# Kernel tuning notes

Measured on AMD Instinct MI355X. Metric: run time of the kernel, lower is better.

Reference implementation:

```python
import jax, jax.numpy as jnp
from jax import lax
import numpy as np

WIN_SIZE = 11
WIN_SIGMA = 1.5
DATA_RANGE = 1.0
K1, K2 = 0.01, 0.03
DN = ('NCHW', 'OIHW', 'NCHW')


def _gauss_1d(size, sigma):
    coords = jnp.arange(size, dtype=jnp.float32) - (size // 2)
    g = jnp.exp(-coords ** 2 / (2.0 * sigma ** 2))
    return g / g.sum()


def _gaussian_filter(x, g):
    # depthwise separable valid conv: along W then along H (order irrelevant)
    C = x.shape[1]
    kw = jnp.tile(g.reshape(1, 1, 1, -1), (C, 1, 1, 1))  # [C,1,1,K]
    kh = jnp.tile(g.reshape(1, 1, -1, 1), (C, 1, 1, 1))  # [C,1,K,1]
    x = lax.conv_general_dilated(x, kw, (1, 1), 'VALID',
                                 feature_group_count=C, dimension_numbers=DN)
    x = lax.conv_general_dilated(x, kh, (1, 1), 'VALID',
                                 feature_group_count=C, dimension_numbers=DN)
    return x


def setup_inputs() -> dict:
    key = jax.random.key(0)
    k1, k2 = jax.random.split(key)
    X = jax.random.uniform(k1, (32, 3, 512, 512), dtype=jnp.float32, minval=-1.0, maxval=1.0)
    Y = jax.random.uniform(k2, (32, 3, 512, 512), dtype=jnp.float32, minval=-1.0, maxval=1.0)
    return {"X": X, "Y": Y}


def reference(X, Y):
    # channel == 3 -> normalize from [-1,1] to [0,1]
    X = (X + 1.0) / 2.0
    Y = (Y + 1.0) / 2.0

    g = _gauss_1d(WIN_SIZE, WIN_SIGMA).astype(X.dtype)
    C1 = (K1 * DATA_RANGE) ** 2
    C2 = (K2 * DATA_RANGE) ** 2

    mu1 = _gaussian_filter(X, g)
    mu2 = _gaussian_filter(Y, g)
    mu1_sq = mu1 * mu1
    mu2_sq = mu2 * mu2
    mu1_mu2 = mu1 * mu2

    sigma1_sq = _gaussian_filter(X * X, g) - mu1_sq
    sigma2_sq = _gaussian_filter(Y * Y, g) - mu2_sq
    sigma12 = _gaussian_filter(X * Y, g) - mu1_mu2

    cs_map = (2.0 * sigma12 + C2) / (sigma1_sq + sigma2_sq + C2)
    ssim_map = (2.0 * mu1_mu2 + C1) / (mu1_sq + mu2_sq + C1) * cs_map

    # size_average=True, full=False -> scalar mean SSIM
    return ssim_map.mean()
```

## Files before the change

### kernel.cpp

```cpp
#include <hip/hip_runtime.h>
#include <cmath>


#define HH 512
#define WW 512
#define OH 502
#define OW 502
#define NC 96
#define TXS 32
#define TYB 30
#define INR 40
#define INRS 42
#define RAWP 13
#define NRAW (INR*RAWP)
#define HP4 33
#define GX 16
#define GY 17
#define NSLOT 64

typedef float f4 __attribute__((ext_vector_type(4)));

struct GaussW { float g[11]; };

static __device__ __forceinline__ f4 sp(float s) { return (f4){s, s, s, s}; }

__global__ __launch_bounds__(256, 4) void ssim_kernel(
        const float* __restrict__ X, const float* __restrict__ Y,
        double* __restrict__ acc, GaussW gw) {
    __shared__ f4 rawS[2 * NRAW];
    __shared__ f4 hS[INRS][HP4];
    __shared__ double wsum[4];

    const int tid = threadIdx.x;
    const int R0 = blockIdx.y * TYB;
    const int C0 = blockIdx.x * TXS;
    const float* Xp = X + (size_t)blockIdx.z * (HH * WW);
    const float* Yp = Y + (size_t)blockIdx.z * (HH * WW);

    #pragma unroll
    for (int k = 0; k < 5; ++k) {
        int i = (k << 8) + tid;
        if (i < 2 * NRAW) {
            int a  = i >= NRAW;
            int j  = a ? i - NRAW : i;
            int r  = j / RAWP;
            int c4 = j - r * RAWP;
            const float* bp  = a ? Yp : Xp;
            const float* src = bp + min(R0 + r, HH - 1) * WW
                                  + min(C0 + 4 * c4, WW - 4);
            f4* dst = &rawS[i & ~63];
            __builtin_amdgcn_global_load_lds(
                (const __attribute__((address_space(1))) void*)src,
                (__attribute__((address_space(3))) void*)dst, 16, 0, 0);
        }
    }
    __syncthreads();

    auto task = [&](int r, int cg) {
        const int ib = RAWP * r + cg;
        f4 x0 = rawS[ib + 0], x1 = rawS[ib + 1];
        f4 x2 = rawS[ib + 2], x3 = rawS[ib + 3];
        f4 y0 = rawS[NRAW + ib + 0], y1 = rawS[NRAW + ib + 1];
        f4 y2 = rawS[NRAW + ib + 2], y3 = rawS[NRAW + ib + 3];
        float xv[16], yv[16];
        #pragma unroll
        for (int i = 0; i < 4; ++i) {
            xv[i] = x0[i]; xv[4 + i] = x1[i]; xv[8 + i] = x2[i]; xv[12 + i] = x3[i];
            yv[i] = y0[i]; yv[4 + i] = y1[i]; yv[8 + i] = y2[i]; yv[12 + i] = y3[i];
        }
        f4 a0v = sp(0.f), a1v = sp(0.f), a2v = sp(0.f), a3v = sp(0.f);
        #pragma unroll
        for (int k = 0; k < 14; ++k) {
            float x = xv[k], y = yv[k];
            f4 P;
            P.x = x; P.y = y;
            P.z = fmaf(x, x, y * y);
            P.w = x * y;
            #pragma unroll
            for (int j = 0; j < 4; ++j) {
                int u = k - j;
                if (u >= 0 && u < 11) {
                    f4 G = sp(gw.g[u]);
                    if (j == 0) a0v = __builtin_elementwise_fma(G, P, a0v);
                    if (j == 1) a1v = __builtin_elementwise_fma(G, P, a1v);
                    if (j == 2) a2v = __builtin_elementwise_fma(G, P, a2v);
                    if (j == 3) a3v = __builtin_elementwise_fma(G, P, a3v);
                }
            }
        }
        hS[r][4 * cg + 0] = a0v;
        hS[r][4 * cg + 1] = a1v;
        hS[r][4 * cg + 2] = a2v;
        hS[r][4 * cg + 3] = a3v;
    };
    {
        const int cg = (tid >> 3) & 7;
        task((tid & 7) | ((tid >> 6) << 3), cg);
        if (tid < 64) task((tid & 7) | 32, cg);
    }
    __syncthreads();

    const int c  = tid & 31;
    const int rb = (tid >> 5) * 4;
    f4 A[4];
    #pragma unroll
    for (int j = 0; j < 4; ++j) A[j] = sp(0.f);
    #pragma unroll
    for (int k = 0; k < 14; ++k) {
        f4 v = hS[rb + k][c];
        #pragma unroll
        for (int j = 0; j < 4; ++j) {
            int u = k - j;
            if (u >= 0 && u < 11) {
                f4 G = sp(gw.g[u]);
                A[j] = __builtin_elementwise_fma(G, v, A[j]);
            }
        }
    }

    const float C1 = 1.0e-4f;
    const float C2 = 9.0e-4f;
    float nn[4], dd[4];
    #pragma unroll
    for (int j = 0; j < 4; ++j) {
        f4 v = A[j];
        float t1 = v.x + 1.f, t2 = v.y + 1.f;
        float num1 = fmaf(t1 * t2, 0.5f, C1);
        float den1 = fmaf(fmaf(t2, t2, t1 * t1), 0.25f, C1);
        float num2 = fmaf(v.w - v.x * v.y, 0.5f, C2);
        float den2 = fmaf(v.z - fmaf(v.x, v.x, v.y * v.y), 0.25f, C2);
        bool valid = (rb + j < TYB) & (R0 + rb + j < OH) & (C0 + c < OW);
        nn[j] = valid ? num1 * num2 : 0.f;
        dd[j] = valid ? den1 * den2 : 1.f;
    }
    float d01 = dd[0] * dd[1], d23 = dd[2] * dd[3];
    float s01 = fmaf(nn[0], dd[1], nn[1] * dd[0]);
    float s23 = fmaf(nn[2], dd[3], nn[3] * dd[2]);
    double tsum = (double)(fmaf(s01, d23, s23 * d01) / (d01 * d23));

    #pragma unroll
    for (int off = 32; off > 0; off >>= 1)
        tsum += __shfl_down(tsum, off, 64);
    if ((tid & 63) == 0) wsum[tid >> 6] = tsum;
    __syncthreads();
    if (tid == 0) {
        int slot = (blockIdx.x + blockIdx.y * GX + blockIdx.z * GX * GY) & (NSLOT - 1);
        atomicAdd(&acc[slot * 8], wsum[0] + wsum[1] + wsum[2] + wsum[3]);
    }
}

__global__ void ssim_finalize(const double* __restrict__ acc,
                              float* __restrict__ out) {
    int lane = threadIdx.x;
    double t = acc[lane * 8];
    #pragma unroll
    for (int off = 32; off > 0; off >>= 1)
        t += __shfl_down(t, off, 64);
    if (lane == 0)
        out[0] = (float)(t * (1.0 / (double)((long long)NC * OH * OW)));
}

extern "C" void kernel_launch(void* const* d_in, const int* in_sizes, int n_in,
                              void* d_out, int out_size, void* d_ws, size_t ws_size,
                              hipStream_t stream) {
    const float* X = (const float*)d_in[0];
    const float* Y = (const float*)d_in[1];
    float* out = (float*)d_out;
    double* acc = (double*)d_ws;

    hipMemsetAsync(d_ws, 0, NSLOT * 64, stream);

    GaussW gw;
    {
        double g[11], s = 0.0;
        for (int i = 0; i < 11; ++i) {
            double d = (double)(i - 5);
            g[i] = exp(-d * d / (2.0 * 1.5 * 1.5));
            s += g[i];
        }
        for (int i = 0; i < 11; ++i) gw.g[i] = (float)(g[i] / s);
    }

    dim3 grid(GX, GY, NC);
    ssim_kernel<<<grid, dim3(256), 0, stream>>>(X, Y, acc, gw);
    ssim_finalize<<<1, dim3(64), 0, stream>>>(acc, out);
}
```

Before: 261.7 us.

## Stream column strips through persistent blocks with double-buffered DMA and ring-buffered halo

Each block now walks down a whole 32-column strip of one image in 16 iterations instead of handling a single 30-row tile. Raw rows are double-buffered through LDS with async global-to-LDS loads for the next batch issued while the current batch is filtered. A circular horizontal-result buffer keeps the 10-row halo between iterations, so overlapping input rows are no longer reloaded and re-filtered. This cuts redundant halo traffic and the halo horizontal pass, but the grid shrinks from 16x17x96 to 16x96 blocks, which lowers parallelism, and each iteration adds barriers.

```diff
diff --git a/kernel.cpp b/kernel.cpp
--- a/kernel.cpp
+++ b/kernel.cpp
@@ -8,14 +8,13 @@
 #define OW 502
 #define NC 96
 #define TXS 32
-#define TYB 30
-#define INR 40
-#define INRS 42
+#define BROWS 32
+#define NIT 16
+#define RAWR 64
 #define RAWP 13
-#define NRAW (INR*RAWP)
+#define HSR 48
 #define HP4 33
 #define GX 16
-#define GY 17
 #define NSLOT 64
 
 typedef float f4 __attribute__((ext_vector_type(4)));
@@ -23,50 +22,59 @@
 struct GaussW { float g[11]; };
 
 static __device__ __forceinline__ f4 sp(float s) { return (f4){s, s, s, s}; }
+
+#define FENCE() asm volatile("" ::: "memory")
 
 __global__ __launch_bounds__(256, 4) void ssim_kernel(
         const float* __restrict__ X, const float* __restrict__ Y,
         double* __restrict__ acc, GaussW gw) {
-    __shared__ f4 rawS[2 * NRAW];
-    __shared__ f4 hS[INRS][HP4];
+    __shared__ f4 rawS[2 * RAWR * RAWP];
+    __shared__ f4 hS[HSR][HP4];
     __shared__ double wsum[4];
 
     const int tid = threadIdx.x;
-    const int R0 = blockIdx.y * TYB;
     const int C0 = blockIdx.x * TXS;
-    const float* Xp = X + (size_t)blockIdx.z * (HH * WW);
-    const float* Yp = Y + (size_t)blockIdx.z * (HH * WW);
-
-    #pragma unroll
-    for (int k = 0; k < 5; ++k) {
-        int i = (k << 8) + tid;
-        if (i < 2 * NRAW) {
-            int a  = i >= NRAW;
-            int j  = a ? i - NRAW : i;
-            int r  = j / RAWP;
-            int c4 = j - r * RAWP;
-            const float* bp  = a ? Yp : Xp;
-            const float* src = bp + min(R0 + r, HH - 1) * WW
-                                  + min(C0 + 4 * c4, WW - 4);
-            f4* dst = &rawS[i & ~63];
-            __builtin_amdgcn_global_load_lds(
-                (const __attribute__((address_space(1))) void*)src,
-                (__attribute__((address_space(3))) void*)dst, 16, 0, 0);
-        }
-    }
-    __syncthreads();
-
-    auto task = [&](int r, int cg) {
-        const int ib = RAWP * r + cg;
+    const float* Xp = X + (size_t)blockIdx.y * (HH * WW);
+    const float* Yp = Y + (size_t)blockIdx.y * (HH * WW);
+
+    auto dma1 = [&](int a, int slot_f4, int row, int c4) {
+        const float* bp  = a ? Yp : Xp;
+        const float* src = bp + (size_t)min(row, HH - 1) * WW
+                              + min(C0 + 4 * c4, WW - 4);
+        f4* dst = rawS + a * (RAWR * RAWP) + slot_f4;
+        __builtin_amdgcn_global_load_lds(
+            (const __attribute__((address_space(1))) void*)src,
+            (__attribute__((address_space(3))) void*)dst, 16, 0, 0);
+    };
+
+    auto dma_batch = [&](int i) {
+        const int half = (i & 1) * (BROWS * RAWP);
+        const int br = 32 * i + 42;
+        #pragma unroll
+        for (int a = 0; a < 2; ++a)
+            #pragma unroll
+            for (int k = 0; k < 2; ++k) {
+                int idx = (k << 8) + tid;
+                if (idx < BROWS * RAWP) {
+                    int o = idx / 13, c4 = idx - o * 13;
+                    dma1(a, half + (k << 8) + (tid & ~63), br + o, c4);
+                }
+            }
+    };
+
+    auto htask = [&](int o, int cg, int rbm, int bm) {
+        const int rs = rbm + o;
+        int hs = bm + o; if (hs >= HSR) hs -= HSR;
+        const int ib = rs * RAWP + cg;
         f4 x0 = rawS[ib + 0], x1 = rawS[ib + 1];
         f4 x2 = rawS[ib + 2], x3 = rawS[ib + 3];
-        f4 y0 = rawS[NRAW + ib + 0], y1 = rawS[NRAW + ib + 1];
-        f4 y2 = rawS[NRAW + ib + 2], y3 = rawS[NRAW + ib + 3];
+        f4 y0 = rawS[RAWR * RAWP + ib + 0], y1 = rawS[RAWR * RAWP + ib + 1];
+        f4 y2 = rawS[RAWR * RAWP + ib + 2], y3 = rawS[RAWR * RAWP + ib + 3];
         float xv[16], yv[16];
         #pragma unroll
-        for (int i = 0; i < 4; ++i) {
-            xv[i] = x0[i]; xv[4 + i] = x1[i]; xv[8 + i] = x2[i]; xv[12 + i] = x3[i];
-            yv[i] = y0[i]; yv[4 + i] = y1[i]; yv[8 + i] = y2[i]; yv[12 + i] = y3[i];
+        for (int q = 0; q < 4; ++q) {
+            xv[q] = x0[q]; xv[4 + q] = x1[q]; xv[8 + q] = x2[q]; xv[12 + q] = x3[q];
+            yv[q] = y0[q]; yv[4 + q] = y1[q]; yv[8 + q] = y2[q]; yv[12 + q] = y3[q];
         }
         f4 a0v = sp(0.f), a1v = sp(0.f), a2v = sp(0.f), a3v = sp(0.f);
         #pragma unroll
@@ -88,55 +96,92 @@
                 }
             }
         }
-        hS[r][4 * cg + 0] = a0v;
-        hS[r][4 * cg + 1] = a1v;
-        hS[r][4 * cg + 2] = a2v;
-        hS[r][4 * cg + 3] = a3v;
+        hS[hs][4 * cg + 0] = a0v;
+        hS[hs][4 * cg + 1] = a1v;
+        hS[hs][4 * cg + 2] = a2v;
+        hS[hs][4 * cg + 3] = a3v;
     };
-    {
-        const int cg = (tid >> 3) & 7;
-        task((tid & 7) | ((tid >> 6) << 3), cg);
-        if (tid < 64) task((tid & 7) | 32, cg);
-    }
-    __syncthreads();
-
+
+    #pragma unroll
+    for (int a = 0; a < 2; ++a)
+        #pragma unroll
+        for (int k = 0; k < 3; ++k) {
+            int idx = (k << 8) + tid;
+            if (idx < 42 * RAWP) {
+                int o = idx / 13, c4 = idx - o * 13;
+                dma1(a, 22 * RAWP + (k << 8) + (tid & ~63), o, c4);
+            }
+        }
+    asm volatile("s_waitcnt vmcnt(0)" ::: "memory");
+    __builtin_amdgcn_s_barrier();
+    FENCE();
+
+    double tsum = 0.0;
     const int c  = tid & 31;
     const int rb = (tid >> 5) * 4;
-    f4 A[4];
-    #pragma unroll
-    for (int j = 0; j < 4; ++j) A[j] = sp(0.f);
-    #pragma unroll
-    for (int k = 0; k < 14; ++k) {
-        f4 v = hS[rb + k][c];
+    int bm = 0;
+    int vb = 0;
+
+    for (int i = 0; i < NIT; ++i) {
+        if (i >= 1 && i <= 14) dma_batch(i);
+
+        const int rbm = (i == 0) ? 22 : (((i + 1) & 1) << 5);
+        {
+            const int cg = (tid >> 3) & 7;
+            const int o  = (tid & 7) | ((tid >> 6) << 3);
+            htask(o, cg, rbm, bm);
+            if (i == 0) {
+                if (tid < 64) htask(32 + (tid & 7), (tid >> 3) & 7, rbm, bm);
+                if (tid < 16) htask(40 + (tid & 1), (tid >> 1) & 7, rbm, bm);
+            }
+        }
+        asm volatile("s_waitcnt lgkmcnt(0)" ::: "memory");
+        __builtin_amdgcn_s_barrier();
+        FENCE();
+        if (i == 0) dma_batch(0);
+        f4 A[4];
+        #pragma unroll
+        for (int j = 0; j < 4; ++j) A[j] = sp(0.f);
+        #pragma unroll
+        for (int k = 0; k < 14; ++k) {
+            int s = vb + rb + k; if (s >= HSR) s -= HSR;
+            f4 v = hS[s][c];
+            #pragma unroll
+            for (int j = 0; j < 4; ++j) {
+                int u = k - j;
+                if (u >= 0 && u < 11) {
+                    f4 G = sp(gw.g[u]);
+                    A[j] = __builtin_elementwise_fma(G, v, A[j]);
+                }
+            }
+        }
+        const float C1 = 1.0e-4f;
+        const float C2 = 9.0e-4f;
+        float nn[4], dd[4];
         #pragma unroll
         for (int j = 0; j < 4; ++j) {
-            int u = k - j;
-            if (u >= 0 && u < 11) {
-                f4 G = sp(gw.g[u]);
-                A[j] = __builtin_elementwise_fma(G, v, A[j]);
-            }
-        }
+            f4 v = A[j];
+            float t1 = v.x + 1.f, t2 = v.y + 1.f;
+            float num1 = fmaf(t1 * t2, 0.5f, C1);
+            float den1 = fmaf(fmaf(t2, t2, t1 * t1), 0.25f, C1);
+            float num2 = fmaf(v.w - v.x * v.y, 0.5f, C2);
+            float den2 = fmaf(v.z - fmaf(v.x, v.x, v.y * v.y), 0.25f, C2);
+            bool valid = (32 * i + rb + j < OH) & (C0 + c < OW);
+            nn[j] = valid ? num1 * num2 : 0.f;
+            dd[j] = valid ? den1 * den2 : 1.f;
+        }
+        float d01 = dd[0] * dd[1], d23 = dd[2] * dd[3];
+        float s01 = fmaf(nn[0], dd[1], nn[1] * dd[0]);
+        float s23 = fmaf(nn[2], dd[3], nn[3] * dd[2]);
+        tsum += (double)(fmaf(s01, d23, s23 * d01) / (d01 * d23));
+
+        asm volatile("s_waitcnt vmcnt(0) lgkmcnt(0)" ::: "memory");
+        __builtin_amdgcn_s_barrier();
+        FENCE();
+
+        bm = (i == 0) ? 42 : (bm + 32 >= HSR ? bm + 32 - HSR : bm + 32);
+        vb = (vb + 32 >= HSR) ? vb + 32 - HSR : vb + 32;
     }
-
-    const float C1 = 1.0e-4f;
-    const float C2 = 9.0e-4f;
-    float nn[4], dd[4];
-    #pragma unroll
-    for (int j = 0; j < 4; ++j) {
-        f4 v = A[j];
-        float t1 = v.x + 1.f, t2 = v.y + 1.f;
-        float num1 = fmaf(t1 * t2, 0.5f, C1);
-        float den1 = fmaf(fmaf(t2, t2, t1 * t1), 0.25f, C1);
-        float num2 = fmaf(v.w - v.x * v.y, 0.5f, C2);
-        float den2 = fmaf(v.z - fmaf(v.x, v.x, v.y * v.y), 0.25f, C2);
-        bool valid = (rb + j < TYB) & (R0 + rb + j < OH) & (C0 + c < OW);
-        nn[j] = valid ? num1 * num2 : 0.f;
-        dd[j] = valid ? den1 * den2 : 1.f;
-    }
-    float d01 = dd[0] * dd[1], d23 = dd[2] * dd[3];
-    float s01 = fmaf(nn[0], dd[1], nn[1] * dd[0]);
-    float s23 = fmaf(nn[2], dd[3], nn[3] * dd[2]);
-    double tsum = (double)(fmaf(s01, d23, s23 * d01) / (d01 * d23));
 
     #pragma unroll
     for (int off = 32; off > 0; off >>= 1)
@@ -144,7 +189,7 @@
     if ((tid & 63) == 0) wsum[tid >> 6] = tsum;
     __syncthreads();
     if (tid == 0) {
-        int slot = (blockIdx.x + blockIdx.y * GX + blockIdx.z * GX * GY) & (NSLOT - 1);
+        int slot = (blockIdx.x + blockIdx.y * GX) & (NSLOT - 1);
         atomicAdd(&acc[slot * 8], wsum[0] + wsum[1] + wsum[2] + wsum[3]);
     }
 }
@@ -181,7 +226,7 @@
         for (int i = 0; i < 11; ++i) gw.g[i] = (float)(g[i] / s);
     }
 
-    dim3 grid(GX, GY, NC);
+    dim3 grid(GX, NC);
     ssim_kernel<<<grid, dim3(256), 0, stream>>>(X, Y, acc, gw);
     ssim_finalize<<<1, dim3(64), 0, stream>>>(acc, out);
 }
```

Measured after the change: 252.4 us. -3.6%, faster.
